# Kernel tuning notes

Hardware: AMD Instinct MI355X
Metric: run time of the kernel (lower is better)

Reference implementation:

```python
import jax, jax.numpy as jnp
import numpy as np

B, S, DMODEL, HEADS = 2, 2048, 1024, 16
DK = DMODEL // HEADS
DV = DMODEL // HEADS


def setup_inputs() -> dict:
    key = jax.random.key(0)
    kx, kq, kk, kv = jax.random.split(key, 4)
    x = jax.random.normal(kx, (B, S, DMODEL), dtype=jnp.float32)
    # stacked per-head projection weights, shape [H, dmodel, dk/dv]
    # (equivalent to nn.Linear(dmodel, dk, bias=False) per head)
    scale = 1.0 / np.sqrt(DMODEL)
    Wq = jax.random.uniform(kq, (HEADS, DMODEL, DK), jnp.float32, -scale, scale)
    Wk = jax.random.uniform(kk, (HEADS, DMODEL, DK), jnp.float32, -scale, scale)
    Wv = jax.random.uniform(kv, (HEADS, DMODEL, DV), jnp.float32, -scale, scale)
    return {"x": x, "Wq": Wq, "Wk": Wk, "Wv": Wv}


def reference(x, Wq, Wk, Wv):
    # per-head projections, batched across heads: [B,H,S,dk]
    q = jnp.einsum("bsd,hdk->bhsk", x, Wq)
    k = jnp.einsum("bsd,hdk->bhsk", x, Wk)
    v = jnp.einsum("bsd,hdv->bhsv", x, Wv)
    # NOTE: original module applies NO 1/sqrt(dk) scaling — keep faithful
    scores = jnp.einsum("bhqk,bhsk->bhqs", q, k)  # [B,H,S,S]
    attn = jax.nn.softmax(scores, axis=-1)
    out = jnp.einsum("bhqs,bhsv->bhqv", attn, v)  # [B,H,S,dv]
    # concat heads along last dim in head order
    Bsz, H, Sq, Dv = out.shape
    return jnp.transpose(out, (0, 2, 1, 3)).reshape(Bsz, Sq, H * Dv)
```

## Files before the change

### kernel.cpp

```cpp
#include <hip/hip_runtime.h>

#define B_ 2
#define S_ 2048
#define D_ 1024
#define H_ 16
#define DK_ 64
#define M_ (B_ * S_)
#define N_ (3 * D_)

typedef __bf16 bf16x8 __attribute__((ext_vector_type(8)));
typedef short s8vec __attribute__((ext_vector_type(8)));
typedef float f4vec __attribute__((ext_vector_type(4)));
typedef float f16vec __attribute__((ext_vector_type(16)));

static __device__ __forceinline__ ushort f2b(float f) {
  union { float f; unsigned u; } v; v.f = f;
  unsigned u = v.u;
  u += 0x7FFFu + ((u >> 16) & 1u);
  return (ushort)(u >> 16);
}

static __device__ __forceinline__ unsigned pk2(float a, float b) {
#if __has_builtin(__builtin_amdgcn_cvt_pk_bf16_f32)
  typedef __bf16 b2 __attribute__((ext_vector_type(2)));
  b2 r = __builtin_amdgcn_cvt_pk_bf16_f32(a, b);
  return __builtin_bit_cast(unsigned, r);
#else
  return (unsigned)f2b(a) | ((unsigned)f2b(b) << 16);
#endif
}

static __device__ __forceinline__ float exp2f_fast(float x) {
#if __has_builtin(__builtin_amdgcn_exp2f)
  return __builtin_amdgcn_exp2f(x);
#else
  return __expf(x * 0.6931471805599453f);
#endif
}

static __device__ __forceinline__ f4vec mfma16(s8vec a, s8vec b, f4vec c) {
  return __builtin_amdgcn_mfma_f32_16x16x32_bf16(
      __builtin_bit_cast(bf16x8, a), __builtin_bit_cast(bf16x8, b), c, 0, 0, 0);
}

static __device__ __forceinline__ f16vec mfma32(s8vec a, s8vec b, f16vec c) {
  return __builtin_amdgcn_mfma_f32_32x32x16_bf16(
      __builtin_bit_cast(bf16x8, a), __builtin_bit_cast(bf16x8, b), c, 0, 0, 0);
}

static __device__ __forceinline__ void gl_lds16(const ushort* g, ushort* l) {
  __builtin_amdgcn_global_load_lds(
      (const __attribute__((address_space(1))) unsigned*)g,
      (__attribute__((address_space(3))) unsigned*)l, 16, 0, 0);
}

static __device__ __forceinline__ void wg_barrier_lds() {
  asm volatile("" ::: "memory");
  __builtin_amdgcn_s_waitcnt(0xC07F);
  __builtin_amdgcn_s_barrier();
  asm volatile("" ::: "memory");
}

__global__ __launch_bounds__(256) void cvt_xw(const float* __restrict__ x,
                                              const float* __restrict__ Wq,
                                              const float* __restrict__ Wk,
                                              const float* __restrict__ Wv,
                                              ushort* __restrict__ xb,
                                              ushort* __restrict__ wbt) {
  __shared__ ushort T[64 * 72];
  const int t = threadIdx.x;
  if (blockIdx.x < 4096) {
    int i = blockIdx.x * 256 + t;
    float4 v = ((const float4*)x)[i];
    ushort4 o;
    o.x = f2b(v.x); o.y = f2b(v.y); o.z = f2b(v.z); o.w = f2b(v.w);
    ((ushort4*)xb)[i] = o;
    return;
  }
  const int r = blockIdx.x - 4096;
  const int w = r >> 8, h = (r >> 4) & 15, d0 = (r & 15) * 64;
  const float* W = (w == 0) ? Wq : (w == 1) ? Wk : Wv;
  const float sc = (w == 0) ? 1.4426950408889634f : 1.0f;
  const float* src = W + (size_t)h * 65536 + (size_t)d0 * 64;
#pragma unroll
  for (int j = 0; j < 4; ++j) {
    int idx = j * 256 + t;
    int dr = idx >> 4, kc = (idx & 15) * 4;
    float4 v = *(const float4*)(src + dr * 64 + kc);
    T[(kc + 0) * 72 + dr] = f2b(v.x * sc);
    T[(kc + 1) * 72 + dr] = f2b(v.y * sc);
    T[(kc + 2) * 72 + dr] = f2b(v.z * sc);
    T[(kc + 3) * 72 + dr] = f2b(v.w * sc);
  }
  __syncthreads();
  const int kk = t >> 2, dcg = (t & 3) * 16;
  ushort* dst = wbt + ((size_t)w * 1024 + h * 64 + kk) * 1024 + d0 + dcg;
  *(s8vec*)dst       = *(const s8vec*)&T[kk * 72 + dcg];
  *(s8vec*)(dst + 8) = *(const s8vec*)&T[kk * 72 + dcg + 8];
}

__global__ __launch_bounds__(512) void proj_gemm(const ushort* __restrict__ xb,
                                                 const ushort* __restrict__ wbt,
                                                 ushort* __restrict__ qkv) {
  __shared__ __attribute__((aligned(16))) ushort As[2][256 * 64];
  __shared__ __attribute__((aligned(16))) ushort Bs[2][192 * 64];
  const int tid = threadIdx.x, wid = tid >> 6, lane = tid & 63;
  const int quad = lane >> 4, l15 = lane & 15;
  const int wm = wid & 1, wn = wid >> 1;
  const int m0 = blockIdx.x * 256, n0 = blockIdx.y * 192;

  f4vec acc[8][3];
#pragma unroll
  for (int mb = 0; mb < 8; mb++)
#pragma unroll
    for (int nb = 0; nb < 3; nb++)
#pragma unroll
      for (int i = 0; i < 4; i++) acc[mb][nb][i] = 0.f;

  const int sr = tid >> 3, sg = tid & 7;
  const int gk = sg ^ (sr & 7);
  const ushort* Ab = xb + (size_t)m0 * D_;
  const ushort* Bb = wbt + (size_t)n0 * D_;

#define PSTAGE(buf, k0_)                                                    \
  do {                                                                      \
    _Pragma("unroll")                                                       \
    for (int j = 0; j < 4; ++j)                                             \
      gl_lds16(Ab + (size_t)(j * 64 + sr) * D_ + (k0_) + gk * 8,            \
               &As[buf][(j * 64 + wid * 8) * 64]);                          \
    _Pragma("unroll")                                                       \
    for (int j = 0; j < 3; ++j)                                             \
      gl_lds16(Bb + (size_t)(j * 64 + sr) * D_ + (k0_) + gk * 8,            \
               &Bs[buf][(j * 64 + wid * 8) * 64]);                          \
  } while (0)

#define PCOMP(buf)                                                          \
  do {                                                                      \
    _Pragma("unroll")                                                       \
    for (int kb = 0; kb < 2; ++kb) {                                        \
      s8vec af[8], bf[3];                                                   \
      _Pragma("unroll")                                                     \
      for (int mb = 0; mb < 8; ++mb) {                                      \
        int m = wm * 128 + mb * 16 + l15;                                   \
        int gpos = (kb * 4 + quad) ^ (m & 7);                               \
        af[mb] = *(const s8vec*)&As[buf][m * 64 + gpos * 8];                \
      }                                                                     \
      _Pragma("unroll")                                                     \
      for (int nb = 0; nb < 3; ++nb) {                                      \
        int n = wn * 48 + nb * 16 + l15;                                    \
        int gpos = (kb * 4 + quad) ^ (n & 7);                               \
        bf[nb] = *(const s8vec*)&Bs[buf][n * 64 + gpos * 8];                \
      }                                                                     \
      _Pragma("unroll")                                                     \
      for (int mb = 0; mb < 8; ++mb)                                        \
        _Pragma("unroll")                                                   \
        for (int nb = 0; nb < 3; ++nb)                                      \
          acc[mb][nb] = mfma16(af[mb], bf[nb], acc[mb][nb]);                \
    }                                                                       \
  } while (0)

  PSTAGE(0, 0);
  __syncthreads();
  for (int t = 0; t < 15; ++t) {
    const int cur = t & 1;
    PSTAGE(cur ^ 1, (t + 1) * 64);
    PCOMP(cur);
    __syncthreads();
  }
  PCOMP(1);
#undef PSTAGE
#undef PCOMP

  const size_t per = (size_t)B_ * H_ * S_ * DK_;
  ushort* vt = qkv + 2 * per;
#pragma unroll
  for (int mb = 0; mb < 8; ++mb)
#pragma unroll
    for (int nb = 0; nb < 3; ++nb) {
      const int n1g = n0 + wn * 48 + nb * 16 + l15;
      const int w = n1g >> 10, n1 = n1g & 1023;
      if (w == 2) {
#pragma unroll
        for (int i = 0; i < 4; ++i) {
          int m = m0 + wm * 128 + mb * 16 + quad * 4 + i;
          int b = m >> 11, s = m & 2047;
          vt[((size_t)b * 1024 + n1) * S_ + s] = f2b(acc[mb][nb][i]);
        }
      } else {
#pragma unroll
        for (int i = 0; i < 4; ++i) {
          int m = m0 + wm * 128 + mb * 16 + quad * 4 + i;
          int b = m >> 11, s = m & 2047;
          qkv[(size_t)w * per + (((size_t)b * H_ + (n1 >> 6)) * S_ + s) * 64 + (n1 & 63)] =
              f2b(acc[mb][nb][i]);
        }
      }
    }
}

__global__ __launch_bounds__(512) void attn(const ushort* __restrict__ qg,
                                            const ushort* __restrict__ kg,
                                            const ushort* __restrict__ vtg,
                                            float* __restrict__ out) {
  __shared__ __attribute__((aligned(16))) ushort KV[128 * 64 + 2 * 64 * 64];
  __shared__ float LM[4][64];
  ushort* Ks  = KV;
  ushort* Vt0 = KV + 128 * 64;
  float*  OM  = (float*)KV;

  const int qt = blockIdx.x, bh = blockIdx.y;
  const int b = bh >> 4, h = bh & 15;
  const int tid = threadIdx.x, wid = tid >> 6, lane = tid & 63;
  const int l31 = lane & 31, hi = lane >> 5, l7 = lane & 7;
  const int qgi = wid >> 1, kh = wid & 1;

  const ushort* qb = qg + ((size_t)bh * S_ + qt * 256 + qgi * 64) * DK_;
  s8vec bq[2][4];
#pragma unroll
  for (int qs = 0; qs < 2; ++qs)
#pragma unroll
    for (int s = 0; s < 4; ++s)
      bq[qs][s] = *(const s8vec*)(qb + (size_t)(qs * 32 + l31) * DK_ + s * 16 + hi * 8);

  f16vec o[2][2];
  float lsum[2] = {0.f, 0.f};
#pragma unroll
  for (int dvh = 0; dvh < 2; ++dvh)
#pragma unroll
    for (int qs = 0; qs < 2; ++qs)
#pragma unroll
      for (int i = 0; i < 16; ++i) o[dvh][qs][i] = 0.f;

  const int r6 = tid >> 3, gs = tid & 7;
  const int gk = gs ^ (r6 & 7);
  const ushort* kb_ = kg + (size_t)bh * S_ * DK_;
  const ushort* vb_ = vtg + (size_t)bh * 64 * S_ + (size_t)r6 * S_;

  s8vec kr[2], vr[2];
  kr[0] = *(const s8vec*)(kb_ + (size_t)r6 * DK_ + gk * 8);
  kr[1] = *(const s8vec*)(kb_ + (size_t)(64 + r6) * DK_ + gk * 8);
  vr[0] = *(const s8vec*)(vb_ + gk * 8);
  vr[1] = *(const s8vec*)(vb_ + 64 + gk * 8);

  for (int kt = 0; kt < S_ / 128; ++kt) {
    wg_barrier_lds();
    *(s8vec*)&Ks[r6 * 64 + gs * 8]        = kr[0];
    *(s8vec*)&Ks[(64 + r6) * 64 + gs * 8] = kr[1];
    *(s8vec*)&Vt0[r6 * 64 + gs * 8]       = vr[0];
    *(s8vec*)&Vt0[4096 + r6 * 64 + gs * 8] = vr[1];
    if (kt + 1 < S_ / 128) {
      const ushort* kn = kb_ + (size_t)(kt + 1) * 128 * DK_;
      kr[0] = *(const s8vec*)(kn + (size_t)r6 * DK_ + gk * 8);
      kr[1] = *(const s8vec*)(kn + (size_t)(64 + r6) * DK_ + gk * 8);
      const ushort* vn = vb_ + (kt + 1) * 128;
      vr[0] = *(const s8vec*)(vn + gk * 8);
      vr[1] = *(const s8vec*)(vn + 64 + gk * 8);
    }
    wg_barrier_lds();

#pragma unroll
    for (int c = 0; c < 2; ++c) {
      const int row0 = kh * 64 + c * 32 + l31;
      s8vec ak[4];
#pragma unroll
      for (int s = 0; s < 4; ++s)
        ak[s] = *(const s8vec*)&Ks[row0 * 64 + (((2 * s + hi)) ^ l7) * 8];

      f16vec st[2];
#pragma unroll
      for (int qs = 0; qs < 2; ++qs)
#pragma unroll
        for (int i = 0; i < 16; ++i) st[qs][i] = 0.f;
#pragma unroll
      for (int s = 0; s < 4; ++s) {
        st[0] = mfma32(ak[s], bq[0][s], st[0]);
        st[1] = mfma32(ak[s], bq[1][s], st[1]);
      }

#pragma unroll
      for (int qs = 0; qs < 2; ++qs) {
        float p[16];
#pragma unroll
        for (int r = 0; r < 16; ++r) p[r] = exp2f_fast(st[qs][r]);
        float s0 = ((p[0] + p[1]) + (p[2] + p[3])) + ((p[4] + p[5]) + (p[6] + p[7]));
        float s1 = ((p[8] + p[9]) + (p[10] + p[11])) + ((p[12] + p[13]) + (p[14] + p[15]));
        lsum[qs] += s0 + s1;
#pragma unroll
        for (int m = 0; m < 2; ++m) {
          unsigned u01 = pk2(p[m * 8 + 0], p[m * 8 + 1]);
          unsigned u23 = pk2(p[m * 8 + 2], p[m * 8 + 3]);
          unsigned u89 = pk2(p[m * 8 + 4], p[m * 8 + 5]);
          unsigned uAB = pk2(p[m * 8 + 6], p[m * 8 + 7]);
          asm("v_permlane32_swap_b32 %0, %1" : "+v"(u01), "+v"(u89));
          asm("v_permlane32_swap_b32 %0, %1" : "+v"(u23), "+v"(uAB));
          union { unsigned u[4]; s8vec v; } pb;
          pb.u[0] = u01;
          pb.u[1] = u23;
          pb.u[2] = u89;
          pb.u[3] = uAB;
#pragma unroll
          for (int dvh = 0; dvh < 2; ++dvh) {
            s8vec av = *(const s8vec*)&Vt0[kh * 4096 + (dvh * 32 + l31) * 64 +
                                           ((4 * c + 2 * m + hi) ^ l7) * 8];
            o[dvh][qs] = mfma32(av, pb.v, o[dvh][qs]);
          }
        }
      }
    }
  }

#pragma unroll
  for (int qs = 0; qs < 2; ++qs) lsum[qs] += __shfl_xor(lsum[qs], 32, 64);

  __syncthreads();
#pragma unroll
  for (int rnd = 0; rnd < 2; ++rnd) {
    if (kh == 1 && (qgi >> 1) == rnd) {
      const int slot = (qgi & 1) * 4;
#pragma unroll
      for (int dvh = 0; dvh < 2; ++dvh)
#pragma unroll
        for (int qs = 0; qs < 2; ++qs)
#pragma unroll
          for (int r = 0; r < 16; ++r)
            OM[(slot + dvh * 2 + qs) * 1024 + r * 64 + lane] = o[dvh][qs][r];
      if (!hi) {
        LM[qgi][l31]      = lsum[0];
        LM[qgi][32 + l31] = lsum[1];
      }
    }
    __syncthreads();
    if (kh == 0 && (qgi >> 1) == rnd) {
      const int slot = (qgi & 1) * 4;
      float linv[2];
#pragma unroll
      for (int qs = 0; qs < 2; ++qs)
        linv[qs] = 1.0f / (lsum[qs] + LM[qgi][qs * 32 + l31]);
      float* ob = out + ((size_t)b * S_ + qt * 256 + qgi * 64) * D_ + h * DK_;
#pragma unroll
      for (int dvh = 0; dvh < 2; ++dvh)
#pragma unroll
        for (int qs = 0; qs < 2; ++qs)
#pragma unroll
          for (int qd = 0; qd < 4; ++qd) {
            float4 vv;
            vv.x = (o[dvh][qs][qd * 4 + 0] +
                    OM[(slot + dvh * 2 + qs) * 1024 + (qd * 4 + 0) * 64 + lane]) * linv[qs];
            vv.y = (o[dvh][qs][qd * 4 + 1] +
                    OM[(slot + dvh * 2 + qs) * 1024 + (qd * 4 + 1) * 64 + lane]) * linv[qs];
            vv.z = (o[dvh][qs][qd * 4 + 2] +
                    OM[(slot + dvh * 2 + qs) * 1024 + (qd * 4 + 2) * 64 + lane]) * linv[qs];
            vv.w = (o[dvh][qs][qd * 4 + 3] +
                    OM[(slot + dvh * 2 + qs) * 1024 + (qd * 4 + 3) * 64 + lane]) * linv[qs];
            *(float4*)&ob[(size_t)(qs * 32 + l31) * D_ + dvh * 32 + qd * 8 + 4 * hi] = vv;
          }
    }
    __syncthreads();
  }
}

extern "C" void kernel_launch(void* const* d_in, const int* in_sizes, int n_in,
                              void* d_out, int out_size, void* d_ws, size_t ws_size,
                              hipStream_t stream) {
  const float* x  = (const float*)d_in[0];
  const float* Wq = (const float*)d_in[1];
  const float* Wk = (const float*)d_in[2];
  const float* Wv = (const float*)d_in[3];
  float* out = (float*)d_out;

  ushort* xb  = (ushort*)d_ws;
  ushort* wbt = xb + (size_t)B_ * S_ * D_;
  ushort* qkv = wbt + (size_t)3 * D_ * D_;
  const size_t per = (size_t)B_ * H_ * S_ * DK_;

  cvt_xw<<<4096 + 768, 256, 0, stream>>>(x, Wq, Wk, Wv, xb, wbt);
  proj_gemm<<<dim3(M_ / 256, N_ / 192), 512, 0, stream>>>(xb, wbt, qkv);
  attn<<<dim3(S_ / 256, B_ * H_), 512, 0, stream>>>(qkv, qkv + per, qkv + 2 * per, out);
}
```

Baseline: 162.2 us.

## Double-buffer K/V tiles with direct global-to-LDS loads and halve the attention query tile

The attention kernel now stages K and V^T tiles straight from global memory into LDS with global_load_lds, using two LDS buffers so the next tile loads while the current one is computed. This replaces the register-staged loads and the two barriers per iteration with a single barrier. The query tile per block drops from 256 to 128 rows (32 per wave instead of 64), which doubles the grid to 512 blocks and cuts accumulator registers. In exchange, each K/V tile is reused by fewer queries, so K/V traffic doubles, and LDS use doubles, which may limit how many blocks fit per CU.

Result: slower. 169.0 us (+4.2%).

```diff
diff --git a/kernel.cpp b/kernel.cpp
--- a/kernel.cpp
+++ b/kernel.cpp
@@ -52,13 +52,6 @@
   __builtin_amdgcn_global_load_lds(
       (const __attribute__((address_space(1))) unsigned*)g,
       (__attribute__((address_space(3))) unsigned*)l, 16, 0, 0);
-}
-
-static __device__ __forceinline__ void wg_barrier_lds() {
-  asm volatile("" ::: "memory");
-  __builtin_amdgcn_s_waitcnt(0xC07F);
-  __builtin_amdgcn_s_barrier();
-  asm volatile("" ::: "memory");
 }
 
 __global__ __launch_bounds__(256) void cvt_xw(const float* __restrict__ x,
@@ -202,11 +195,9 @@
                                             const ushort* __restrict__ kg,
                                             const ushort* __restrict__ vtg,
                                             float* __restrict__ out) {
-  __shared__ __attribute__((aligned(16))) ushort KV[128 * 64 + 2 * 64 * 64];
-  __shared__ float LM[4][64];
-  ushort* Ks  = KV;
-  ushort* Vt0 = KV + 128 * 64;
-  float*  OM  = (float*)KV;
+  __shared__ __attribute__((aligned(16))) ushort POOL[2][128 * 64 + 2 * 64 * 64];
+  __shared__ float LM[4][32];
+  float* OM = (float*)POOL;
 
   const int qt = blockIdx.x, bh = blockIdx.y;
   const int b = bh >> 4, h = bh & 15;
@@ -214,148 +205,109 @@
   const int l31 = lane & 31, hi = lane >> 5, l7 = lane & 7;
   const int qgi = wid >> 1, kh = wid & 1;
 
-  const ushort* qb = qg + ((size_t)bh * S_ + qt * 256 + qgi * 64) * DK_;
-  s8vec bq[2][4];
-#pragma unroll
-  for (int qs = 0; qs < 2; ++qs)
-#pragma unroll
-    for (int s = 0; s < 4; ++s)
-      bq[qs][s] = *(const s8vec*)(qb + (size_t)(qs * 32 + l31) * DK_ + s * 16 + hi * 8);
-
-  f16vec o[2][2];
-  float lsum[2] = {0.f, 0.f};
+  const ushort* qb = qg + ((size_t)bh * S_ + qt * 128 + qgi * 32) * DK_;
+  s8vec bq[4];
+#pragma unroll
+  for (int s = 0; s < 4; ++s)
+    bq[s] = *(const s8vec*)(qb + (size_t)l31 * DK_ + s * 16 + hi * 8);
+
+  f16vec o[2];
+  float lsum = 0.f;
 #pragma unroll
   for (int dvh = 0; dvh < 2; ++dvh)
 #pragma unroll
-    for (int qs = 0; qs < 2; ++qs)
-#pragma unroll
-      for (int i = 0; i < 16; ++i) o[dvh][qs][i] = 0.f;
-
-  const int r6 = tid >> 3, gs = tid & 7;
-  const int gk = gs ^ (r6 & 7);
+    for (int i = 0; i < 16; ++i) o[dvh][i] = 0.f;
+
+  const int srow = wid * 8 + (lane >> 3);
+  const int gk = (lane & 7) ^ ((lane >> 3) & 7);
   const ushort* kb_ = kg + (size_t)bh * S_ * DK_;
-  const ushort* vb_ = vtg + (size_t)bh * 64 * S_ + (size_t)r6 * S_;
-
-  s8vec kr[2], vr[2];
-  kr[0] = *(const s8vec*)(kb_ + (size_t)r6 * DK_ + gk * 8);
-  kr[1] = *(const s8vec*)(kb_ + (size_t)(64 + r6) * DK_ + gk * 8);
-  vr[0] = *(const s8vec*)(vb_ + gk * 8);
-  vr[1] = *(const s8vec*)(vb_ + 64 + gk * 8);
+  const ushort* vb_ = vtg + (size_t)bh * 64 * S_ + (size_t)srow * S_;
+
+#define STAGE(buf, kt_)                                                     \
+  do {                                                                      \
+    const ushort* kk0 = kb_ + (size_t)((kt_) * 128 + srow) * DK_ + gk * 8;  \
+    gl_lds16(kk0, &POOL[buf][wid * 512]);                                   \
+    gl_lds16(kk0 + (size_t)64 * DK_, &POOL[buf][4096 + wid * 512]);         \
+    gl_lds16(vb_ + (kt_) * 128 + gk * 8, &POOL[buf][8192 + wid * 512]);     \
+    gl_lds16(vb_ + (kt_) * 128 + 64 + gk * 8,                               \
+             &POOL[buf][8192 + 4096 + wid * 512]);                          \
+  } while (0)
+
+  STAGE(0, 0);
+  __syncthreads();
 
   for (int kt = 0; kt < S_ / 128; ++kt) {
-    wg_barrier_lds();
-    *(s8vec*)&Ks[r6 * 64 + gs * 8]        = kr[0];
-    *(s8vec*)&Ks[(64 + r6) * 64 + gs * 8] = kr[1];
-    *(s8vec*)&Vt0[r6 * 64 + gs * 8]       = vr[0];
-    *(s8vec*)&Vt0[4096 + r6 * 64 + gs * 8] = vr[1];
-    if (kt + 1 < S_ / 128) {
-      const ushort* kn = kb_ + (size_t)(kt + 1) * 128 * DK_;
-      kr[0] = *(const s8vec*)(kn + (size_t)r6 * DK_ + gk * 8);
-      kr[1] = *(const s8vec*)(kn + (size_t)(64 + r6) * DK_ + gk * 8);
-      const ushort* vn = vb_ + (kt + 1) * 128;
-      vr[0] = *(const s8vec*)(vn + gk * 8);
-      vr[1] = *(const s8vec*)(vn + 64 + gk * 8);
-    }
-    wg_barrier_lds();
-
+    const int cur = kt & 1;
+    if (kt + 1 < S_ / 128) STAGE(cur ^ 1, kt + 1);
+
+    const ushort* ksb = POOL[cur];
+    const ushort* vtb = POOL[cur] + 8192;
 #pragma unroll
     for (int c = 0; c < 2; ++c) {
       const int row0 = kh * 64 + c * 32 + l31;
       s8vec ak[4];
 #pragma unroll
       for (int s = 0; s < 4; ++s)
-        ak[s] = *(const s8vec*)&Ks[row0 * 64 + (((2 * s + hi)) ^ l7) * 8];
-
-      f16vec st[2];
-#pragma unroll
-      for (int qs = 0; qs < 2; ++qs)
-#pragma unroll
-        for (int i = 0; i < 16; ++i) st[qs][i] = 0.f;
-#pragma unroll
-      for (int s = 0; s < 4; ++s) {
-        st[0] = mfma32(ak[s], bq[0][s], st[0]);
-        st[1] = mfma32(ak[s], bq[1][s], st[1]);
-      }
-
-#pragma unroll
-      for (int qs = 0; qs < 2; ++qs) {
-        float p[16];
-#pragma unroll
-        for (int r = 0; r < 16; ++r) p[r] = exp2f_fast(st[qs][r]);
-        float s0 = ((p[0] + p[1]) + (p[2] + p[3])) + ((p[4] + p[5]) + (p[6] + p[7]));
-        float s1 = ((p[8] + p[9]) + (p[10] + p[11])) + ((p[12] + p[13]) + (p[14] + p[15]));
-        lsum[qs] += s0 + s1;
-#pragma unroll
-        for (int m = 0; m < 2; ++m) {
-          unsigned u01 = pk2(p[m * 8 + 0], p[m * 8 + 1]);
-          unsigned u23 = pk2(p[m * 8 + 2], p[m * 8 + 3]);
-          unsigned u89 = pk2(p[m * 8 + 4], p[m * 8 + 5]);
-          unsigned uAB = pk2(p[m * 8 + 6], p[m * 8 + 7]);
-          asm("v_permlane32_swap_b32 %0, %1" : "+v"(u01), "+v"(u89));
-          asm("v_permlane32_swap_b32 %0, %1" : "+v"(u23), "+v"(uAB));
-          union { unsigned u[4]; s8vec v; } pb;
-          pb.u[0] = u01;
-          pb.u[1] = u23;
-          pb.u[2] = u89;
-          pb.u[3] = uAB;
-#pragma unroll
-          for (int dvh = 0; dvh < 2; ++dvh) {
-            s8vec av = *(const s8vec*)&Vt0[kh * 4096 + (dvh * 32 + l31) * 64 +
-                                           ((4 * c + 2 * m + hi) ^ l7) * 8];
-            o[dvh][qs] = mfma32(av, pb.v, o[dvh][qs]);
-          }
+        ak[s] = *(const s8vec*)&ksb[row0 * 64 + ((2 * s + hi) ^ l7) * 8];
+
+      f16vec st;
+#pragma unroll
+      for (int i = 0; i < 16; ++i) st[i] = 0.f;
+#pragma unroll
+      for (int s = 0; s < 4; ++s) st = mfma32(ak[s], bq[s], st);
+
+      float p[16];
+#pragma unroll
+      for (int r = 0; r < 16; ++r) p[r] = exp2f_fast(st[r]);
+      lsum += (((p[0] + p[1]) + (p[2] + p[3])) + ((p[4] + p[5]) + (p[6] + p[7]))) +
+              (((p[8] + p[9]) + (p[10] + p[11])) + ((p[12] + p[13]) + (p[14] + p[15])));
+#pragma unroll
+      for (int m = 0; m < 2; ++m) {
+        unsigned u01 = pk2(p[m * 8 + 0], p[m * 8 + 1]);
+        unsigned u23 = pk2(p[m * 8 + 2], p[m * 8 + 3]);
+        unsigned u89 = pk2(p[m * 8 + 4], p[m * 8 + 5]);
+        unsigned uAB = pk2(p[m * 8 + 6], p[m * 8 + 7]);
+        asm("v_permlane32_swap_b32 %0, %1" : "+v"(u01), "+v"(u89));
+        asm("v_permlane32_swap_b32 %0, %1" : "+v"(u23), "+v"(uAB));
+        union { unsigned u[4]; s8vec v; } pb;
+        pb.u[0] = u01; pb.u[1] = u23; pb.u[2] = u89; pb.u[3] = uAB;
+#pragma unroll
+        for (int dvh = 0; dvh < 2; ++dvh) {
+          s8vec av = *(const s8vec*)&vtb[kh * 4096 + (dvh * 32 + l31) * 64 +
+                                         ((4 * c + 2 * m + hi) ^ l7) * 8];
+          o[dvh] = mfma32(av, pb.v, o[dvh]);
         }
       }
     }
-  }
-
-#pragma unroll
-  for (int qs = 0; qs < 2; ++qs) lsum[qs] += __shfl_xor(lsum[qs], 32, 64);
-
+    __syncthreads();
+  }
+#undef STAGE
+
+  lsum += __shfl_xor(lsum, 32, 64);
+
+  if (kh == 1) {
+#pragma unroll
+    for (int dvh = 0; dvh < 2; ++dvh)
+#pragma unroll
+      for (int r = 0; r < 16; ++r)
+        OM[(qgi * 2 + dvh) * 2048 + r * 64 + lane] = o[dvh][r];
+    if (!hi) LM[qgi][l31] = lsum;
+  }
   __syncthreads();
-#pragma unroll
-  for (int rnd = 0; rnd < 2; ++rnd) {
-    if (kh == 1 && (qgi >> 1) == rnd) {
-      const int slot = (qgi & 1) * 4;
-#pragma unroll
-      for (int dvh = 0; dvh < 2; ++dvh)
-#pragma unroll
-        for (int qs = 0; qs < 2; ++qs)
-#pragma unroll
-          for (int r = 0; r < 16; ++r)
-            OM[(slot + dvh * 2 + qs) * 1024 + r * 64 + lane] = o[dvh][qs][r];
-      if (!hi) {
-        LM[qgi][l31]      = lsum[0];
-        LM[qgi][32 + l31] = lsum[1];
+  if (kh == 0) {
+    const float linv = 1.0f / (lsum + LM[qgi][l31]);
+    float* ob = out + ((size_t)b * S_ + qt * 128 + qgi * 32) * D_ + h * DK_;
+#pragma unroll
+    for (int dvh = 0; dvh < 2; ++dvh)
+#pragma unroll
+      for (int qd = 0; qd < 4; ++qd) {
+        float4 vv;
+        vv.x = (o[dvh][qd * 4 + 0] + OM[(qgi * 2 + dvh) * 2048 + (qd * 4 + 0) * 64 + lane]) * linv;
+        vv.y = (o[dvh][qd * 4 + 1] + OM[(qgi * 2 + dvh) * 2048 + (qd * 4 + 1) * 64 + lane]) * linv;
+        vv.z = (o[dvh][qd * 4 + 2] + OM[(qgi * 2 + dvh) * 2048 + (qd * 4 + 2) * 64 + lane]) * linv;
+        vv.w = (o[dvh][qd * 4 + 3] + OM[(qgi * 2 + dvh) * 2048 + (qd * 4 + 3) * 64 + lane]) * linv;
+        *(float4*)&ob[(size_t)l31 * D_ + dvh * 32 + qd * 8 + 4 * hi] = vv;
       }
-    }
-    __syncthreads();
-    if (kh == 0 && (qgi >> 1) == rnd) {
-      const int slot = (qgi & 1) * 4;
-      float linv[2];
-#pragma unroll
-      for (int qs = 0; qs < 2; ++qs)
-        linv[qs] = 1.0f / (lsum[qs] + LM[qgi][qs * 32 + l31]);
-      float* ob = out + ((size_t)b * S_ + qt * 256 + qgi * 64) * D_ + h * DK_;
-#pragma unroll
-      for (int dvh = 0; dvh < 2; ++dvh)
-#pragma unroll
-        for (int qs = 0; qs < 2; ++qs)
-#pragma unroll
-          for (int qd = 0; qd < 4; ++qd) {
-            float4 vv;
-            vv.x = (o[dvh][qs][qd * 4 + 0] +
-                    OM[(slot + dvh * 2 + qs) * 1024 + (qd * 4 + 0) * 64 + lane]) * linv[qs];
-            vv.y = (o[dvh][qs][qd * 4 + 1] +
-                    OM[(slot + dvh * 2 + qs) * 1024 + (qd * 4 + 1) * 64 + lane]) * linv[qs];
-            vv.z = (o[dvh][qs][qd * 4 + 2] +
-                    OM[(slot + dvh * 2 + qs) * 1024 + (qd * 4 + 2) * 64 + lane]) * linv[qs];
-            vv.w = (o[dvh][qs][qd * 4 + 3] +
-                    OM[(slot + dvh * 2 + qs) * 1024 + (qd * 4 + 3) * 64 + lane]) * linv[qs];
-            *(float4*)&ob[(size_t)(qs * 32 + l31) * D_ + dvh * 32 + qd * 8 + 4 * hi] = vv;
-          }
-    }
-    __syncthreads();
   }
 }
 
@@ -375,5 +327,5 @@
 
   cvt_xw<<<4096 + 768, 256, 0, stream>>>(x, Wq, Wk, Wv, xb, wbt);
   proj_gemm<<<dim3(M_ / 256, N_ / 192), 512, 0, stream>>>(xb, wbt, qkv);
-  attn<<<dim3(S_ / 256, B_ * H_), 512, 0, stream>>>(qkv, qkv + per, qkv + 2 * per, out);
-}
+  attn<<<dim3(S_ / 128, B_ * H_), 512, 0, stream>>>(qkv, qkv + per, qkv + 2 * per, out);
+}
```
